# Performance work log

Hardware: AMD Instinct MI355X
Metric: run time of the kernel (lower is better)

Reference implementation:

```python
import jax, jax.numpy as jnp
import numpy as np


def _ln(x, g, b, eps=1e-5):
    m = x.mean(-1, keepdims=True)
    v = x.var(-1, keepdims=True)
    return (x - m) / jnp.sqrt(v + eps) * g + b


def setup_inputs() -> dict:
    key = jax.random.key(0)
    ks = jax.random.split(key, 10)
    N, H, E, OUT, L = 4096, 256, 131072, 64, 6
    s = 1.0 / np.sqrt(H)
    return {
        "x": jax.random.normal(ks[0], (N, H), jnp.float32),
        "edge_index": jax.random.randint(ks[1], (2, E), 0, N, jnp.int32),
        "sage_wl": jax.random.normal(ks[2], (L, H, H), jnp.float32) * s,   # lin_l (neighbors, has bias)
        "sage_wr": jax.random.normal(ks[3], (L, H, H), jnp.float32) * s,   # lin_r (root, no bias)
        "sage_bl": jnp.zeros((L, H), jnp.float32),
        "ln_g": jnp.ones((L - 1, H), jnp.float32),
        "ln_b": jnp.zeros((L - 1, H), jnp.float32),
        "conv_w": jax.random.normal(ks[4], (3, H, H, 3), jnp.float32) * (1.0 / np.sqrt(3 * H)),  # [layer,O,I,K]
        "conv_b": jnp.zeros((3, H), jnp.float32),
        "cnorm_g": jnp.ones((3, H), jnp.float32),
        "cnorm_b": jnp.zeros((3, H), jnp.float32),
        "in_proj_w": jax.random.normal(ks[5], (6 * H, 2 * H), jnp.float32) * (1.0 / np.sqrt(2 * H)),
        "in_proj_b": jnp.zeros((6 * H,), jnp.float32),
        "out_proj_w": jax.random.normal(ks[6], (2 * H, 2 * H), jnp.float32) * (1.0 / np.sqrt(2 * H)),
        "out_proj_b": jnp.zeros((2 * H,), jnp.float32),
        "anorm_g": jnp.ones((2 * H,), jnp.float32),
        "anorm_b": jnp.zeros((2 * H,), jnp.float32),
        "fuse_w": jax.random.normal(ks[7], (OUT, 2 * H), jnp.float32) * (1.0 / np.sqrt(2 * H)),
        "fuse_b": jnp.zeros((OUT,), jnp.float32),
    }


def reference(x, edge_index, sage_wl, sage_wr, sage_bl, ln_g, ln_b,
              conv_w, conv_b, cnorm_g, cnorm_b,
              in_proj_w, in_proj_b, out_proj_w, out_proj_b,
              anorm_g, anorm_b, fuse_w, fuse_b):
    # Dropout layers act as identity (eval mode).
    N, H = x.shape
    L = sage_wl.shape[0]
    src, dst = edge_index[0], edge_index[1]
    deg = jax.ops.segment_sum(jnp.ones(src.shape[0], x.dtype), dst, num_segments=N)
    deg = jnp.maximum(deg, 1.0)[:, None]
    h = x
    for i in range(L):
        res = h
        # SAGEConv: mean-aggregate neighbor features (gather/scatter), then two linears
        agg = jax.ops.segment_sum(h[src], dst, num_segments=N) / deg
        h = agg @ sage_wl[i].T + sage_bl[i] + h @ sage_wr[i].T
        if i < L - 1:
            h = _ln(h, ln_g[i], ln_b[i])
        h = jax.nn.relu(h) + res  # residual (shapes always match: in==hidden)
    gnn_out = h                                   # [N, H]

    # CNN branch over the node axis: [1, H, N]
    c = gnn_out.T[None]
    for j in range(3):
        c = jax.lax.conv_general_dilated(c, conv_w[j], (1,), ((1, 1),),
                                         dimension_numbers=("NCH", "OIH", "NCH"))
        c = jax.nn.relu(c + conv_b[j][None, :, None])
        c = _ln(c.transpose(0, 2, 1), cnorm_g[j], cnorm_b[j]).transpose(0, 2, 1)
    cnn_out = c[0].T                              # [N, H]

    fused = jnp.concatenate([gnn_out, cnn_out], axis=1)  # [N, 2H]
    E2 = fused.shape[1]
    heads = 4
    hd = E2 // heads
    qkv = fused @ in_proj_w.T + in_proj_b
    q, k, v = jnp.split(qkv, 3, axis=1)
    split_heads = lambda t: t.reshape(N, heads, hd).transpose(1, 0, 2)  # [h, N, hd]
    q, k, v = split_heads(q), split_heads(k), split_heads(v)
    scores = jnp.einsum("hnd,hmd->hnm", q, k) / np.sqrt(hd).astype(np.float32)
    a = jax.nn.softmax(scores, axis=-1)
    o = jnp.einsum("hnm,hmd->hnd", a, v).transpose(1, 0, 2).reshape(N, E2)
    o = o @ out_proj_w.T + out_proj_b
    o = _ln(o, anorm_g, anorm_b)
    return o @ fuse_w.T + fuse_b                  # [N, out_channels]
```

## Files before the change

### kernel.cpp

```cpp
#include <hip/hip_runtime.h>

#define NN 4096
#define HH 256
#define EE 131072

__device__ __constant__ float LN_EPS = 1e-5f;
#define ATT_SCALE 0.08838834764831845f
#define ATT_SHIFT 30.0f

typedef __attribute__((ext_vector_type(8))) short bf16x8_t;
typedef __attribute__((ext_vector_type(4))) float f32x4_t;

__device__ inline ushort f2b(float f) {
  uint u = __float_as_uint(f);
  uint r = (u + 0x7FFF + ((u >> 16) & 1)) >> 16;
  return (ushort)r;
}

__global__ void hist_kernel(const int* __restrict__ ei, int* __restrict__ cnt) {
  int e = blockIdx.x * blockDim.x + threadIdx.x;
  if (e < EE) atomicAdd(&cnt[ei[EE + e]], 1);
}

__global__ __launch_bounds__(1024) void scan_kernel(int* __restrict__ cnt_cursor,
                                                    int* __restrict__ rowptr,
                                                    float* __restrict__ invdeg) {
  __shared__ int part[1024];
  int t = threadIdx.x;
  int base = t * 4;
  int cs[4];
  int s = 0;
  for (int u = 0; u < 4; ++u) { cs[u] = cnt_cursor[base + u]; s += cs[u]; }
  part[t] = s;
  __syncthreads();
  for (int off = 1; off < 1024; off <<= 1) {
    int add = (t >= off) ? part[t - off] : 0;
    int v = part[t];
    __syncthreads();
    part[t] = v + add;
    __syncthreads();
  }
  int excl = (t > 0) ? part[t - 1] : 0;
  for (int u = 0; u < 4; ++u) {
    rowptr[base + u] = excl;
    cnt_cursor[base + u] = excl;
    invdeg[base + u] = 1.0f / (float)max(cs[u], 1);
    excl += cs[u];
  }
  if (t == 1023) rowptr[NN] = excl;
}

__global__ void fill_kernel(const int* __restrict__ ei, int* __restrict__ cursor,
                            int* __restrict__ col) {
  int e = blockIdx.x * blockDim.x + threadIdx.x;
  if (e < EE) {
    int d = ei[EE + e];
    int p = atomicAdd(&cursor[d], 1);
    col[p] = ei[e];
  }
}

__global__ __launch_bounds__(256) void castw(const float* __restrict__ in,
                                             ushort* __restrict__ out) {
  int i4 = (blockIdx.x * 256 + threadIdx.x) * 4;
  float4 v = *(const float4*)(in + i4);
  ushort4 w;
  w.x = f2b(v.x); w.y = f2b(v.y); w.z = f2b(v.z); w.w = f2b(v.w);
  *(ushort4*)(out + i4) = w;
}

__global__ __launch_bounds__(256) void castconv(const float* __restrict__ w,
                                                ushort* __restrict__ o) {
  int idx = blockIdx.x * 256 + threadIdx.x;
  int j = idx / 196608;
  int rem = idx - j * 196608;
  int oc = rem / 768;
  int kk = rem - oc * 768;
  int ks = kk >> 8, ii = kk & 255;
  o[idx] = f2b(w[j * 196608 + oc * 768 + ii * 3 + ks]);
}

__global__ __launch_bounds__(64) void agg_kernel(const float* __restrict__ h,
                                                 const int* __restrict__ rowptr,
                                                 const int* __restrict__ col,
                                                 const float* __restrict__ invdeg,
                                                 ushort* __restrict__ aggb) {
  int n = blockIdx.x;
  int t = threadIdx.x;
  int s = rowptr[n], e = rowptr[n + 1];
  float4 acc = make_float4(0.f, 0.f, 0.f, 0.f);
  for (int j = s; j < e; ++j) {
    int c = col[j];
    const float4 v = *(const float4*)(h + (size_t)c * HH + t * 4);
    acc.x += v.x; acc.y += v.y; acc.z += v.z; acc.w += v.w;
  }
  float id = invdeg[n];
  ushort4 w;
  w.x = f2b(acc.x * id); w.y = f2b(acc.y * id);
  w.z = f2b(acc.z * id); w.w = f2b(acc.w * id);
  *(ushort4*)(aggb + (size_t)n * HH + t * 4) = w;
}

__global__ __launch_bounds__(256) void gemm_mfma(
    const ushort* __restrict__ A0, const ushort* __restrict__ A1,
    const ushort* __restrict__ B0, const ushort* __restrict__ B1,
    const float* __restrict__ bias, float* __restrict__ Cf, ushort* __restrict__ Cb,
    int M, int Nn, int K, int KHA, int KHB, int relu) {
  __shared__ ushort Alds[64][40];
  __shared__ ushort Blds[128][40];
  int t = threadIdx.x;
  int w = t >> 6, l = t & 63, quad = l >> 4, lr = l & 15;
  int wm = w & 1, wn = w >> 1;
  int m0 = blockIdx.x * 64, n0 = blockIdx.y * 128;
  int sr = t >> 2, sc8 = (t & 3) * 8;
  f32x4_t acc[2][4];
#pragma unroll
  for (int s = 0; s < 2; ++s)
#pragma unroll
    for (int q = 0; q < 4; ++q) acc[s][q] = (f32x4_t){0.f, 0.f, 0.f, 0.f};

  for (int k0 = 0; k0 < K; k0 += 32) {
    int kk = k0 + sc8;
    const ushort* ap = (kk < KHA) ? (A0 + (size_t)(m0 + sr) * KHA + kk)
                                  : (A1 + (size_t)(m0 + sr) * (K - KHA) + (kk - KHA));
    uint4 av = *(const uint4*)ap;
    const ushort* bp0 = (kk < KHB) ? (B0 + (size_t)(n0 + sr) * KHB + kk)
                                   : (B1 + (size_t)(n0 + sr) * (K - KHB) + (kk - KHB));
    uint4 bv0 = *(const uint4*)bp0;
    const ushort* bp1 = (kk < KHB) ? (B0 + (size_t)(n0 + 64 + sr) * KHB + kk)
                                   : (B1 + (size_t)(n0 + 64 + sr) * (K - KHB) + (kk - KHB));
    uint4 bv1 = *(const uint4*)bp1;
    __syncthreads();
    *(uint4*)&Alds[sr][sc8] = av;
    *(uint4*)&Blds[sr][sc8] = bv0;
    *(uint4*)&Blds[64 + sr][sc8] = bv1;
    __syncthreads();
    bf16x8_t af[2], bf[4];
#pragma unroll
    for (int s = 0; s < 2; ++s)
      af[s] = *(const bf16x8_t*)&Alds[wm * 32 + s * 16 + lr][quad * 8];
#pragma unroll
    for (int q = 0; q < 4; ++q)
      bf[q] = *(const bf16x8_t*)&Blds[wn * 64 + q * 16 + lr][quad * 8];
#pragma unroll
    for (int s = 0; s < 2; ++s)
#pragma unroll
      for (int q = 0; q < 4; ++q)
        acc[s][q] = __builtin_amdgcn_mfma_f32_16x16x32_bf16(af[s], bf[q], acc[s][q], 0, 0, 0);
  }
#pragma unroll
  for (int s = 0; s < 2; ++s) {
#pragma unroll
    for (int q = 0; q < 4; ++q) {
      int n = n0 + wn * 64 + q * 16 + lr;
      float bb = bias[n];
#pragma unroll
      for (int r = 0; r < 4; ++r) {
        int m = m0 + wm * 32 + s * 16 + quad * 4 + r;
        float v = acc[s][q][r] + bb;
        if (relu) v = fmaxf(v, 0.f);
        if (Cf) Cf[(size_t)m * Nn + n] = v;
        if (Cb) Cb[(size_t)m * Nn + n] = f2b(v);
      }
    }
  }
}

__global__ __launch_bounds__(256) void gemm_conv_mfma(
    const ushort* __restrict__ Ab, const ushort* __restrict__ B,
    const float* __restrict__ bias, float* __restrict__ Cf) {
  __shared__ ushort Alds[64][40];
  __shared__ ushort Blds[128][40];
  int t = threadIdx.x;
  int w = t >> 6, l = t & 63, quad = l >> 4, lr = l & 15;
  int wm = w & 1, wn = w >> 1;
  int m0 = blockIdx.x * 64, n0 = blockIdx.y * 128;
  int sr = t >> 2, sc8 = (t & 3) * 8;
  f32x4_t acc[2][4];
#pragma unroll
  for (int s = 0; s < 2; ++s)
#pragma unroll
    for (int q = 0; q < 4; ++q) acc[s][q] = (f32x4_t){0.f, 0.f, 0.f, 0.f};

  for (int k0 = 0; k0 < 768; k0 += 32) {
    int kk = k0 + sc8;
    int ks = kk >> 8, ii = kk & 255;
    int nr = m0 + sr + ks - 1;
    uint4 av = make_uint4(0u, 0u, 0u, 0u);
    if (nr >= 0 && nr < NN) av = *(const uint4*)(Ab + (size_t)nr * HH + ii);
    uint4 bv0 = *(const uint4*)(B + (size_t)(n0 + sr) * 768 + kk);
    uint4 bv1 = *(const uint4*)(B + (size_t)(n0 + 64 + sr) * 768 + kk);
    __syncthreads();
    *(uint4*)&Alds[sr][sc8] = av;
    *(uint4*)&Blds[sr][sc8] = bv0;
    *(uint4*)&Blds[64 + sr][sc8] = bv1;
    __syncthreads();
    bf16x8_t af[2], bf[4];
#pragma unroll
    for (int s = 0; s < 2; ++s)
      af[s] = *(const bf16x8_t*)&Alds[wm * 32 + s * 16 + lr][quad * 8];
#pragma unroll
    for (int q = 0; q < 4; ++q)
      bf[q] = *(const bf16x8_t*)&Blds[wn * 64 + q * 16 + lr][quad * 8];
#pragma unroll
    for (int s = 0; s < 2; ++s)
#pragma unroll
      for (int q = 0; q < 4; ++q)
        acc[s][q] = __builtin_amdgcn_mfma_f32_16x16x32_bf16(af[s], bf[q], acc[s][q], 0, 0, 0);
  }
#pragma unroll
  for (int s = 0; s < 2; ++s) {
#pragma unroll
    for (int q = 0; q < 4; ++q) {
      int n = n0 + wn * 64 + q * 16 + lr;
      float bb = bias[n];
#pragma unroll
      for (int r = 0; r < 4; ++r) {
        int m = m0 + wm * 32 + s * 16 + quad * 4 + r;
        Cf[(size_t)m * HH + n] = fmaxf(acc[s][q][r] + bb, 0.f);
      }
    }
  }
}

__global__ __launch_bounds__(256) void gemm_std(
    const float* __restrict__ A0, const float* __restrict__ B0,
    const float* __restrict__ bias, float* __restrict__ C,
    int M, int Nn, int K) {
  __shared__ float As[16][68];
  __shared__ float Bs[16][68];
  int t = threadIdx.x;
  int m0 = blockIdx.x * 64, n0 = blockIdx.y * 64;
  int ty = t >> 4, tx = t & 15;
  int lr = t >> 2, lc4 = (t & 3) * 4;
  float acc[4][4] = {};
  for (int k0 = 0; k0 < K; k0 += 16) {
    int kk = k0 + lc4;
    float4 va = *(const float4*)(A0 + (size_t)(m0 + lr) * K + kk);
    As[lc4 + 0][lr] = va.x; As[lc4 + 1][lr] = va.y;
    As[lc4 + 2][lr] = va.z; As[lc4 + 3][lr] = va.w;
    float4 vb = *(const float4*)(B0 + (size_t)(n0 + lr) * K + kk);
    Bs[lc4 + 0][lr] = vb.x; Bs[lc4 + 1][lr] = vb.y;
    Bs[lc4 + 2][lr] = vb.z; Bs[lc4 + 3][lr] = vb.w;
    __syncthreads();
#pragma unroll
    for (int k = 0; k < 16; ++k) {
      float4 a4 = *(const float4*)&As[k][4 * ty];
      float4 b4 = *(const float4*)&Bs[k][4 * tx];
      float av[4] = {a4.x, a4.y, a4.z, a4.w};
      float bv[4] = {b4.x, b4.y, b4.z, b4.w};
#pragma unroll
      for (int i = 0; i < 4; ++i)
#pragma unroll
        for (int j = 0; j < 4; ++j) acc[i][j] += av[i] * bv[j];
    }
    __syncthreads();
  }
#pragma unroll
  for (int i = 0; i < 4; ++i) {
    int m = m0 + 4 * ty + i;
    float o[4];
#pragma unroll
    for (int j = 0; j < 4; ++j) o[j] = acc[i][j] + bias[n0 + 4 * tx + j];
    float4 o4 = make_float4(o[0], o[1], o[2], o[3]);
    *(float4*)(C + (size_t)m * Nn + n0 + 4 * tx) = o4;
  }
}

__global__ __launch_bounds__(256) void ln_fuse(
    const float* __restrict__ x, const float* __restrict__ g, const float* __restrict__ b,
    const float* __restrict__ res, float* __restrict__ outf, ushort* __restrict__ outb,
    int D, int do_ln, int relu_res) {
  int row = blockIdx.x, t = threadIdx.x;
  int nv = D >> 8;
  float vals[2];
  float s = 0.f, sq = 0.f;
  for (int u = 0; u < nv; ++u) {
    float v = x[(size_t)row * D + t + (u << 8)];
    vals[u] = v; s += v; sq += v * v;
  }
  __shared__ float red[8];
  float m = 0.f, inv = 1.f;
  if (do_ln) {
    for (int off = 32; off >= 1; off >>= 1) {
      s += __shfl_xor(s, off);
      sq += __shfl_xor(sq, off);
    }
    int wid = t >> 6;
    if ((t & 63) == 0) { red[wid] = s; red[4 + wid] = sq; }
    __syncthreads();
    if (t == 0) {
      float S = red[0] + red[1] + red[2] + red[3];
      float Q = red[4] + red[5] + red[6] + red[7];
      float mm = S / D;
      float vv = Q / D - mm * mm;
      red[0] = mm;
      red[1] = rsqrtf(vv + LN_EPS);
    }
    __syncthreads();
    m = red[0]; inv = red[1];
  }
  for (int u = 0; u < nv; ++u) {
    int c = t + (u << 8);
    float y = vals[u];
    if (do_ln) y = (y - m) * inv * g[c] + b[c];
    if (relu_res) y = fmaxf(y, 0.f) + res[(size_t)row * D + c];
    if (outf) outf[(size_t)row * D + c] = y;
    if (outb) outb[(size_t)row * D + c] = f2b(y);
  }
}

__global__ __launch_bounds__(256) void kvpack(const ushort* __restrict__ qkvb,
                                              ushort* __restrict__ Kt,
                                              ushort* __restrict__ VtT) {
  int t = threadIdx.x;
  int n0 = blockIdx.x * 32;
  int by = blockIdx.y;
  int kt = n0 >> 5;
  {
    int head = by >> 2, ks = by & 3;
    int key = t >> 3, e4 = (t & 7) * 4;
    uint2 v = *(const uint2*)(qkvb + (size_t)(n0 + key) * 1536 + 512 + head * 128 + ks * 32 + e4);
    *(uint2*)(Kt + ((((size_t)head * 128 + kt) * 4 + ks) * 32 + key) * 32 + e4) = v;
  }
  __shared__ ushort tile[32][34];
  int d0 = by * 32;
  int tx = t & 31, ty = t >> 5;
#pragma unroll
  for (int u = 0; u < 4; ++u) {
    int r = ty + 8 * u;
    tile[r][tx] = qkvb[(size_t)(n0 + r) * 1536 + 1024 + d0 + tx];
  }
  __syncthreads();
#pragma unroll
  for (int u = 0; u < 4; ++u) {
    int dg = d0 + ty + 8 * u;
    int head = dg >> 7, dl = dg & 127;
    VtT[((((size_t)head * 128 + kt) * 128 + dl) << 5) + tx] = tile[tx][ty + 8 * u];
  }
}

__global__ __launch_bounds__(256, 2) void attn_mfma(const ushort* __restrict__ qkvb,
                                                    const ushort* __restrict__ Kt,
                                                    const ushort* __restrict__ VtT,
                                                    ushort* __restrict__ Ob) {
  __shared__ __align__(16) char smem[66048];
  int t = threadIdx.x;
  int w = t >> 6, l = t & 63;
  int quad = l >> 4, lr = l & 15;
  int head = blockIdx.y;
  int q0 = blockIdx.x * 32;

  ushort* Pl = (ushort*)smem + w * 1280;

  bf16x8_t qf[2][4];
#pragma unroll
  for (int s = 0; s < 2; ++s)
#pragma unroll
    for (int ks = 0; ks < 4; ++ks)
      qf[s][ks] = *(const bf16x8_t*)(qkvb + (size_t)(q0 + s * 16 + lr) * 1536 +
                                     head * 128 + ks * 32 + quad * 8);

  f32x4_t of[2][8];
#pragma unroll
  for (int s = 0; s < 2; ++s)
#pragma unroll
    for (int dt = 0; dt < 8; ++dt) of[s][dt] = (f32x4_t){0.f, 0.f, 0.f, 0.f};
  float den[2][4] = {{0.f, 0.f, 0.f, 0.f}, {0.f, 0.f, 0.f, 0.f}};

  const int lnoff = lr * 32 + quad * 8;
  const int tile0 = w * 32;

  for (int tt = 0; tt < 32; ++tt) {
    int kt = tile0 + tt;
    const ushort* kbase = Kt + (((size_t)head * 128 + kt) << 12);
    const ushort* vbase = VtT + (((size_t)head * 128 + kt) << 12);

    bf16x8_t kf[4][2];
#pragma unroll
    for (int ks = 0; ks < 4; ++ks)
#pragma unroll
      for (int ct = 0; ct < 2; ++ct)
        kf[ks][ct] = *(const bf16x8_t*)(kbase + ks * 1024 + ct * 512 + lnoff);
    f32x4_t sf[2][2];
#pragma unroll
    for (int s = 0; s < 2; ++s)
#pragma unroll
      for (int ct = 0; ct < 2; ++ct) sf[s][ct] = (f32x4_t){0.f, 0.f, 0.f, 0.f};
#pragma unroll
    for (int ks = 0; ks < 4; ++ks)
#pragma unroll
      for (int ct = 0; ct < 2; ++ct)
#pragma unroll
        for (int s = 0; s < 2; ++s)
          sf[s][ct] = __builtin_amdgcn_mfma_f32_16x16x32_bf16(qf[s][ks], kf[ks][ct], sf[s][ct], 0, 0, 0);

    bf16x8_t vf[8];
#pragma unroll
    for (int dt = 0; dt < 8; ++dt)
      vf[dt] = *(const bf16x8_t*)(vbase + dt * 512 + lnoff);

#pragma unroll
    for (int s = 0; s < 2; ++s)
#pragma unroll
      for (int ct = 0; ct < 2; ++ct)
#pragma unroll
        for (int r = 0; r < 4; ++r) {
          float e = __expf(sf[s][ct][r] * ATT_SCALE - ATT_SHIFT);
          Pl[(s * 16 + quad * 4 + r) * 40 + ct * 16 + lr] = f2b(e);
          den[s][r] += e;
        }

#pragma unroll
    for (int s = 0; s < 2; ++s) {
      bf16x8_t pf = *(const bf16x8_t*)&Pl[(s * 16 + lr) * 40 + quad * 8];
#pragma unroll
      for (int dt = 0; dt < 8; ++dt)
        of[s][dt] = __builtin_amdgcn_mfma_f32_16x16x32_bf16(pf, vf[dt], of[s][dt], 0, 0, 0);
    }
  }

#pragma unroll
  for (int mask = 1; mask < 16; mask <<= 1)
#pragma unroll
    for (int s = 0; s < 2; ++s)
#pragma unroll
      for (int r = 0; r < 4; ++r) den[s][r] += __shfl_xor(den[s][r], mask);

  __syncthreads();
  float* Osum = (float*)smem;
  float* Dsum = (float*)(smem + 65536);
#pragma unroll
  for (int s = 0; s < 2; ++s)
#pragma unroll
    for (int dt = 0; dt < 8; ++dt)
#pragma unroll
      for (int r = 0; r < 4; ++r)
        Osum[w * 4096 + (s * 16 + quad * 4 + r) * 128 + dt * 16 + lr] = of[s][dt][r];
  if (lr == 0) {
#pragma unroll
    for (int s = 0; s < 2; ++s)
#pragma unroll
      for (int r = 0; r < 4; ++r) Dsum[w * 32 + s * 16 + quad * 4 + r] = den[s][r];
  }
  __syncthreads();
#pragma unroll
  for (int e = 0; e < 16; ++e) {
    int idx = l + e * 64;
    int row = w * 8 + (idx >> 7), col = idx & 127;
    float o = Osum[row * 128 + col] + Osum[4096 + row * 128 + col] +
              Osum[8192 + row * 128 + col] + Osum[12288 + row * 128 + col];
    float dn = Dsum[row] + Dsum[32 + row] + Dsum[64 + row] + Dsum[96 + row];
    Ob[(size_t)(q0 + row) * 512 + head * 128 + col] = f2b(o / dn);
  }
}

extern "C" void kernel_launch(void* const* d_in, const int* in_sizes, int n_in,
                              void* d_out, int out_size, void* d_ws, size_t ws_size,
                              hipStream_t stream) {
  const float* x          = (const float*)d_in[0];
  const int*   ei         = (const int*)d_in[1];
  const float* sage_wl    = (const float*)d_in[2];
  const float* sage_wr    = (const float*)d_in[3];
  const float* sage_bl    = (const float*)d_in[4];
  const float* ln_g       = (const float*)d_in[5];
  const float* ln_b       = (const float*)d_in[6];
  const float* conv_w     = (const float*)d_in[7];
  const float* conv_b     = (const float*)d_in[8];
  const float* cnorm_g    = (const float*)d_in[9];
  const float* cnorm_b    = (const float*)d_in[10];
  const float* in_proj_w  = (const float*)d_in[11];
  const float* in_proj_b  = (const float*)d_in[12];
  const float* out_proj_w = (const float*)d_in[13];
  const float* out_proj_b = (const float*)d_in[14];
  const float* anorm_g    = (const float*)d_in[15];
  const float* anorm_b    = (const float*)d_in[16];
  const float* fuse_w     = (const float*)d_in[17];
  const float* fuse_b     = (const float*)d_in[18];
  float* out = (float*)d_out;

  char* ws = (char*)d_ws;
  const size_t MB = 1 << 20;
  int*    rowptr = (int*)(ws + 0);
  int*    cnt    = (int*)(ws + 65536);
  int*    col    = (int*)(ws + 131072);
  float*  invdeg = (float*)(ws + 786432);
  float*  h    = (float*)(ws + 1 * MB);
  ushort* hb   = (ushort*)(ws + 5 * MB);
  ushort* aggb = (ushort*)(ws + 7 * MB);
  float*  tmp  = (float*)(ws + 9 * MB);
  ushort* c0b  = (ushort*)(ws + 13 * MB);
  ushort* c1b  = (ushort*)(ws + 15 * MB);
  ushort* qkvb = (ushort*)(ws + 17 * MB);
  float*  op   = (float*)(ws + 17 * MB);
  ushort* Kt   = (ushort*)(ws + 1 * MB);
  ushort* Vt   = (ushort*)(ws + 29 * MB);
  ushort* aob  = (ushort*)(ws + 33 * MB);
  ushort* wlb  = (ushort*)(ws + 37 * MB);
  ushort* wrb  = (ushort*)(ws + 37 * MB + 786432);
  ushort* cvb  = (ushort*)(ws + 37 * MB + 1572864);
  ushort* ipb  = (ushort*)(ws + 37 * MB + 2752512);
  ushort* opb  = (ushort*)(ws + 37 * MB + 4325376);

  castw<<<(6 * 256 * 256) / 1024, 256, 0, stream>>>(sage_wl, wlb);
  castw<<<(6 * 256 * 256) / 1024, 256, 0, stream>>>(sage_wr, wrb);
  castconv<<<(3 * 256 * 768) / 256, 256, 0, stream>>>(conv_w, cvb);
  castw<<<(1536 * 512) / 1024, 256, 0, stream>>>(in_proj_w, ipb);
  castw<<<(512 * 512) / 1024, 256, 0, stream>>>(out_proj_w, opb);

  hipMemsetAsync(cnt, 0, NN * sizeof(int), stream);
  hist_kernel<<<EE / 256, 256, 0, stream>>>(ei, cnt);
  scan_kernel<<<1, 1024, 0, stream>>>(cnt, rowptr, invdeg);
  fill_kernel<<<EE / 256, 256, 0, stream>>>(ei, cnt, col);
  hipMemcpyAsync(h, x, (size_t)NN * HH * sizeof(float), hipMemcpyDeviceToDevice, stream);
  castw<<<(NN * HH) / 1024, 256, 0, stream>>>(x, hb);

  for (int i = 0; i < 6; ++i) {
    agg_kernel<<<NN, 64, 0, stream>>>(h, rowptr, col, invdeg, aggb);
    gemm_mfma<<<dim3(64, 2), 256, 0, stream>>>(
        aggb, hb, wlb + (size_t)i * HH * HH, wrb + (size_t)i * HH * HH,
        sage_bl + i * HH, tmp, nullptr, NN, HH, 512, 256, 256, 0);
    int do_ln = (i < 5) ? 1 : 0;
    const float* gp = do_ln ? (ln_g + i * HH) : ln_g;
    const float* bp = do_ln ? (ln_b + i * HH) : ln_b;
    ln_fuse<<<NN, 256, 0, stream>>>(tmp, gp, bp, h, h, hb, HH, do_ln, 1);
  }

  const ushort* cin = hb;
  ushort* couts[3] = {c0b, c1b, c0b};
  for (int j = 0; j < 3; ++j) {
    gemm_conv_mfma<<<dim3(64, 2), 256, 0, stream>>>(
        cin, cvb + (size_t)j * HH * 768, conv_b + j * HH, tmp);
    ln_fuse<<<NN, 256, 0, stream>>>(tmp, cnorm_g + j * HH, cnorm_b + j * HH,
                                    nullptr, nullptr, couts[j], HH, 1, 0);
    cin = couts[j];
  }

  gemm_mfma<<<dim3(64, 12), 256, 0, stream>>>(
      hb, c0b, ipb, nullptr, in_proj_b, nullptr, qkvb, NN, 1536, 512, 256, 1536 * 0 + 512, 0);
  kvpack<<<dim3(NN / 32, 16), 256, 0, stream>>>(qkvb, Kt, Vt);
  attn_mfma<<<dim3(NN / 32, 4), 256, 0, stream>>>(qkvb, Kt, Vt, aob);

  gemm_mfma<<<dim3(64, 4), 256, 0, stream>>>(
      aob, nullptr, opb, nullptr, out_proj_b, op, nullptr, NN, 512, 512, 512, 512, 0);
  ln_fuse<<<NN, 256, 0, stream>>>(op, anorm_g, anorm_b, nullptr, op, nullptr, 512, 1, 0);
  gemm_std<<<dim3(64, 1), 256, 0, stream>>>(op, fuse_w, fuse_b, out, NN, 64, 512);
}
```

Measured before the change: 551.6 us.

## Split-K SAGE and conv GEMMs across grid z, prefetch K tiles in attention

The SAGE layer GEMM now runs as two independent half-K GEMMs (neighbor and root paths) on blockIdx.z, and the conv GEMM splits its 768-deep reduction into two halves. Both write partial results that ln_fuse sums, with ReLU moved into ln_fuse for the conv path. This doubles the block count of small 128-block grids so more CUs are busy. The attention kernel double-buffers K fragments in registers and raises wave priority around the MFMA sections, to overlap loads with compute. The cost is an extra fp32 partial buffer to write and read, and more register pressure in attention.

```diff
diff --git a/kernel.cpp b/kernel.cpp
--- a/kernel.cpp
+++ b/kernel.cpp
@@ -166,15 +166,21 @@
   }
 }
 
-__global__ __launch_bounds__(256) void gemm_conv_mfma(
-    const ushort* __restrict__ Ab, const ushort* __restrict__ B,
-    const float* __restrict__ bias, float* __restrict__ Cf) {
+__global__ __launch_bounds__(256) void gemm_dual(
+    const ushort* __restrict__ A0, const ushort* __restrict__ B0,
+    const float* __restrict__ bias0, float* __restrict__ C0,
+    const ushort* __restrict__ A1, const ushort* __restrict__ B1,
+    float* __restrict__ C1) {
   __shared__ ushort Alds[64][40];
   __shared__ ushort Blds[128][40];
   int t = threadIdx.x;
   int w = t >> 6, l = t & 63, quad = l >> 4, lr = l & 15;
   int wm = w & 1, wn = w >> 1;
   int m0 = blockIdx.x * 64, n0 = blockIdx.y * 128;
+  int z = blockIdx.z;
+  const ushort* A = z ? A1 : A0;
+  const ushort* B = z ? B1 : B0;
+  float* C = z ? C1 : C0;
   int sr = t >> 2, sc8 = (t & 3) * 8;
   f32x4_t acc[2][4];
 #pragma unroll
@@ -182,8 +188,64 @@
 #pragma unroll
     for (int q = 0; q < 4; ++q) acc[s][q] = (f32x4_t){0.f, 0.f, 0.f, 0.f};
 
-  for (int k0 = 0; k0 < 768; k0 += 32) {
+  for (int k0 = 0; k0 < 256; k0 += 32) {
     int kk = k0 + sc8;
+    uint4 av = *(const uint4*)(A + (size_t)(m0 + sr) * 256 + kk);
+    uint4 bv0 = *(const uint4*)(B + (size_t)(n0 + sr) * 256 + kk);
+    uint4 bv1 = *(const uint4*)(B + (size_t)(n0 + 64 + sr) * 256 + kk);
+    __syncthreads();
+    *(uint4*)&Alds[sr][sc8] = av;
+    *(uint4*)&Blds[sr][sc8] = bv0;
+    *(uint4*)&Blds[64 + sr][sc8] = bv1;
+    __syncthreads();
+    bf16x8_t af[2], bf[4];
+#pragma unroll
+    for (int s = 0; s < 2; ++s)
+      af[s] = *(const bf16x8_t*)&Alds[wm * 32 + s * 16 + lr][quad * 8];
+#pragma unroll
+    for (int q = 0; q < 4; ++q)
+      bf[q] = *(const bf16x8_t*)&Blds[wn * 64 + q * 16 + lr][quad * 8];
+#pragma unroll
+    for (int s = 0; s < 2; ++s)
+#pragma unroll
+      for (int q = 0; q < 4; ++q)
+        acc[s][q] = __builtin_amdgcn_mfma_f32_16x16x32_bf16(af[s], bf[q], acc[s][q], 0, 0, 0);
+  }
+#pragma unroll
+  for (int s = 0; s < 2; ++s) {
+#pragma unroll
+    for (int q = 0; q < 4; ++q) {
+      int n = n0 + wn * 64 + q * 16 + lr;
+      float bb = z ? 0.f : bias0[n];
+#pragma unroll
+      for (int r = 0; r < 4; ++r) {
+        int m = m0 + wm * 32 + s * 16 + quad * 4 + r;
+        C[(size_t)m * 256 + n] = acc[s][q][r] + bb;
+      }
+    }
+  }
+}
+
+__global__ __launch_bounds__(256) void gemm_conv_mfma(
+    const ushort* __restrict__ Ab, const ushort* __restrict__ B,
+    const float* __restrict__ bias, float* __restrict__ C0, float* __restrict__ C1) {
+  __shared__ ushort Alds[64][40];
+  __shared__ ushort Blds[128][40];
+  int t = threadIdx.x;
+  int w = t >> 6, l = t & 63, quad = l >> 4, lr = l & 15;
+  int wm = w & 1, wn = w >> 1;
+  int m0 = blockIdx.x * 64, n0 = blockIdx.y * 128;
+  int z = blockIdx.z;
+  float* C = z ? C1 : C0;
+  int sr = t >> 2, sc8 = (t & 3) * 8;
+  f32x4_t acc[2][4];
+#pragma unroll
+  for (int s = 0; s < 2; ++s)
+#pragma unroll
+    for (int q = 0; q < 4; ++q) acc[s][q] = (f32x4_t){0.f, 0.f, 0.f, 0.f};
+
+  for (int k0 = 0; k0 < 384; k0 += 32) {
+    int kk = z * 384 + k0 + sc8;
     int ks = kk >> 8, ii = kk & 255;
     int nr = m0 + sr + ks - 1;
     uint4 av = make_uint4(0u, 0u, 0u, 0u);
@@ -213,11 +275,11 @@
 #pragma unroll
     for (int q = 0; q < 4; ++q) {
       int n = n0 + wn * 64 + q * 16 + lr;
-      float bb = bias[n];
+      float bb = z ? 0.f : bias[n];
 #pragma unroll
       for (int r = 0; r < 4; ++r) {
         int m = m0 + wm * 32 + s * 16 + quad * 4 + r;
-        Cf[(size_t)m * HH + n] = fmaxf(acc[s][q][r] + bb, 0.f);
+        C[(size_t)m * HH + n] = acc[s][q][r] + bb;
       }
     }
   }
@@ -268,15 +330,19 @@
 }
 
 __global__ __launch_bounds__(256) void ln_fuse(
-    const float* __restrict__ x, const float* __restrict__ g, const float* __restrict__ b,
+    const float* __restrict__ x, const float* __restrict__ x2,
+    const float* __restrict__ g, const float* __restrict__ b,
     const float* __restrict__ res, float* __restrict__ outf, ushort* __restrict__ outb,
-    int D, int do_ln, int relu_res) {
+    int D, int do_ln, int relu_res, int prerelu) {
   int row = blockIdx.x, t = threadIdx.x;
   int nv = D >> 8;
   float vals[2];
   float s = 0.f, sq = 0.f;
   for (int u = 0; u < nv; ++u) {
-    float v = x[(size_t)row * D + t + (u << 8)];
+    int c = t + (u << 8);
+    float v = x[(size_t)row * D + c];
+    if (x2) v += x2[(size_t)row * D + c];
+    if (prerelu) v = fmaxf(v, 0.f);
     vals[u] = v; s += v; sq += v * v;
   }
   __shared__ float red[8];
@@ -371,34 +437,50 @@
   const int lnoff = lr * 32 + quad * 8;
   const int tile0 = w * 32;
 
+  bf16x8_t kfA[4][2];
+  {
+    const ushort* kb = Kt + (((size_t)head * 128 + tile0) << 12);
+#pragma unroll
+    for (int ks = 0; ks < 4; ++ks)
+#pragma unroll
+      for (int ct = 0; ct < 2; ++ct)
+        kfA[ks][ct] = *(const bf16x8_t*)(kb + ks * 1024 + ct * 512 + lnoff);
+  }
+
+#pragma unroll 2
   for (int tt = 0; tt < 32; ++tt) {
     int kt = tile0 + tt;
-    const ushort* kbase = Kt + (((size_t)head * 128 + kt) << 12);
     const ushort* vbase = VtT + (((size_t)head * 128 + kt) << 12);
-
-    bf16x8_t kf[4][2];
-#pragma unroll
-    for (int ks = 0; ks < 4; ++ks)
-#pragma unroll
-      for (int ct = 0; ct < 2; ++ct)
-        kf[ks][ct] = *(const bf16x8_t*)(kbase + ks * 1024 + ct * 512 + lnoff);
-    f32x4_t sf[2][2];
-#pragma unroll
-    for (int s = 0; s < 2; ++s)
-#pragma unroll
-      for (int ct = 0; ct < 2; ++ct) sf[s][ct] = (f32x4_t){0.f, 0.f, 0.f, 0.f};
-#pragma unroll
-    for (int ks = 0; ks < 4; ++ks)
-#pragma unroll
-      for (int ct = 0; ct < 2; ++ct)
-#pragma unroll
-        for (int s = 0; s < 2; ++s)
-          sf[s][ct] = __builtin_amdgcn_mfma_f32_16x16x32_bf16(qf[s][ks], kf[ks][ct], sf[s][ct], 0, 0, 0);
 
     bf16x8_t vf[8];
 #pragma unroll
     for (int dt = 0; dt < 8; ++dt)
       vf[dt] = *(const bf16x8_t*)(vbase + dt * 512 + lnoff);
+
+    bf16x8_t kfB[4][2];
+    if (tt < 31) {
+      const ushort* kb = Kt + (((size_t)head * 128 + kt + 1) << 12);
+#pragma unroll
+      for (int ks = 0; ks < 4; ++ks)
+#pragma unroll
+        for (int ct = 0; ct < 2; ++ct)
+          kfB[ks][ct] = *(const bf16x8_t*)(kb + ks * 1024 + ct * 512 + lnoff);
+    }
+
+    f32x4_t sf[2][2];
+#pragma unroll
+    for (int s = 0; s < 2; ++s)
+#pragma unroll
+      for (int ct = 0; ct < 2; ++ct) sf[s][ct] = (f32x4_t){0.f, 0.f, 0.f, 0.f};
+    __builtin_amdgcn_s_setprio(1);
+#pragma unroll
+    for (int ks = 0; ks < 4; ++ks)
+#pragma unroll
+      for (int ct = 0; ct < 2; ++ct)
+#pragma unroll
+        for (int s = 0; s < 2; ++s)
+          sf[s][ct] = __builtin_amdgcn_mfma_f32_16x16x32_bf16(qf[s][ks], kfA[ks][ct], sf[s][ct], 0, 0, 0);
+    __builtin_amdgcn_s_setprio(0);
 
 #pragma unroll
     for (int s = 0; s < 2; ++s)
@@ -411,12 +493,21 @@
           den[s][r] += e;
         }
 
+    __builtin_amdgcn_s_setprio(1);
 #pragma unroll
     for (int s = 0; s < 2; ++s) {
       bf16x8_t pf = *(const bf16x8_t*)&Pl[(s * 16 + lr) * 40 + quad * 8];
 #pragma unroll
       for (int dt = 0; dt < 8; ++dt)
         of[s][dt] = __builtin_amdgcn_mfma_f32_16x16x32_bf16(pf, vf[dt], of[s][dt], 0, 0, 0);
+    }
+    __builtin_amdgcn_s_setprio(0);
+
+    if (tt < 31) {
+#pragma unroll
+      for (int ks = 0; ks < 4; ++ks)
+#pragma unroll
+        for (int ct = 0; ct < 2; ++ct) kfA[ks][ct] = kfB[ks][ct];
     }
   }
 
@@ -493,6 +584,7 @@
   ushort* c1b  = (ushort*)(ws + 15 * MB);
   ushort* qkvb = (ushort*)(ws + 17 * MB);
   float*  op   = (float*)(ws + 17 * MB);
+  float*  tmp2 = (float*)(ws + 25 * MB);
   ushort* Kt   = (ushort*)(ws + 1 * MB);
   ushort* Vt   = (ushort*)(ws + 29 * MB);
   ushort* aob  = (ushort*)(ws + 33 * MB);
@@ -517,22 +609,22 @@
 
   for (int i = 0; i < 6; ++i) {
     agg_kernel<<<NN, 64, 0, stream>>>(h, rowptr, col, invdeg, aggb);
-    gemm_mfma<<<dim3(64, 2), 256, 0, stream>>>(
-        aggb, hb, wlb + (size_t)i * HH * HH, wrb + (size_t)i * HH * HH,
-        sage_bl + i * HH, tmp, nullptr, NN, HH, 512, 256, 256, 0);
+    gemm_dual<<<dim3(64, 2, 2), 256, 0, stream>>>(
+        aggb, wlb + (size_t)i * HH * HH, sage_bl + i * HH, tmp,
+        hb, wrb + (size_t)i * HH * HH, tmp2);
     int do_ln = (i < 5) ? 1 : 0;
     const float* gp = do_ln ? (ln_g + i * HH) : ln_g;
     const float* bp = do_ln ? (ln_b + i * HH) : ln_b;
-    ln_fuse<<<NN, 256, 0, stream>>>(tmp, gp, bp, h, h, hb, HH, do_ln, 1);
+    ln_fuse<<<NN, 256, 0, stream>>>(tmp, tmp2, gp, bp, h, h, hb, HH, do_ln, 1, 0);
   }
 
   const ushort* cin = hb;
   ushort* couts[3] = {c0b, c1b, c0b};
   for (int j = 0; j < 3; ++j) {
-    gemm_conv_mfma<<<dim3(64, 2), 256, 0, stream>>>(
-        cin, cvb + (size_t)j * HH * 768, conv_b + j * HH, tmp);
-    ln_fuse<<<NN, 256, 0, stream>>>(tmp, cnorm_g + j * HH, cnorm_b + j * HH,
-                                    nullptr, nullptr, couts[j], HH, 1, 0);
+    gemm_conv_mfma<<<dim3(64, 2, 2), 256, 0, stream>>>(
+        cin, cvb + (size_t)j * HH * 768, conv_b + j * HH, tmp, tmp2);
+    ln_fuse<<<NN, 256, 0, stream>>>(tmp, tmp2, cnorm_g + j * HH, cnorm_b + j * HH,
+                                    nullptr, nullptr, couts[j], HH, 1, 0, 1);
     cin = couts[j];
   }
 
@@ -543,6 +635,6 @@
 
   gemm_mfma<<<dim3(64, 4), 256, 0, stream>>>(
       aob, nullptr, opb, nullptr, out_proj_b, op, nullptr, NN, 512, 512, 512, 512, 0);
-  ln_fuse<<<NN, 256, 0, stream>>>(op, anorm_g, anorm_b, nullptr, op, nullptr, 512, 1, 0);
+  ln_fuse<<<NN, 256, 0, stream>>>(op, nullptr, anorm_g, anorm_b, nullptr, op, nullptr, 512, 1, 0, 0);
   gemm_std<<<dim3(64, 1), 256, 0, stream>>>(op, fuse_w, fuse_b, out, NN, 64, 512);
 }
```

After: 517.6 us. -6.2%, faster.
